# Performance work log

Measured on AMD Instinct MI355X. Metric: run time of the kernel, lower is better.

The kernel has to match this reference:

```python
import jax, jax.numpy as jnp
import numpy as np

N, K, D_INT, D_EXT = 10000, 16, 8, 16
D = 128          # node_representation_size
V_INT = 50000    # unique_internal_nodes
B = 2048


def _xavier(key, shape):
    fan_in, fan_out = shape[-1], shape[-2] if len(shape) > 1 else shape[-1]
    std = float(np.sqrt(2.0 / (fan_in + fan_out)))
    return jax.random.normal(key, shape, dtype=jnp.float32) * std


def setup_inputs() -> dict:
    key = jax.random.key(0)
    ks = jax.random.split(key, 16)
    batch = jax.random.randint(ks[0], (B, 2), 0, N)
    int_node_ids = jax.random.randint(ks[1], (N, K), 0, V_INT)
    int_neigh_ids = jax.random.randint(ks[2], (N, K, D_INT), 0, V_INT)
    ext_neigh = jax.random.randint(ks[3], (N, D_EXT), 0, N)
    E = jax.random.normal(ks[4], (V_INT, D), dtype=jnp.float32)  # nn.Embedding default init
    W = _xavier(ks[5], (D, D))
    M = _xavier(ks[6], (D, D))
    U = _xavier(ks[7], (D, D))
    V = _xavier(ks[8], (D, D))
    W1 = _xavier(ks[9], (D, 2 * D))
    b1 = jnp.zeros((D,), dtype=jnp.float32)
    W2 = _xavier(ks[10], (2, D))
    b2 = jnp.zeros((2,), dtype=jnp.float32)
    return {"batch": batch, "int_node_ids": int_node_ids,
            "int_neigh_ids": int_neigh_ids, "ext_neigh": ext_neigh,
            "E": E, "W": W, "M": M, "U": U, "V": V,
            "W1": W1, "b1": b1, "W2": W2, "b2": b2}


def reference(batch, int_node_ids, int_neigh_ids, ext_neigh,
              E, W, M, U, V, W1, b1, W2, b2):
    # --- InternalGraphConvolutionLayer, vectorized over all N external nodes ---
    emb = E[int_node_ids]                          # (N, K, d) per-internal-node embedding
    nb_sum = E[int_neigh_ids].sum(axis=2)          # (N, K, d) sum of internal neighbours
    # sum_k = relu(W @ e_k + M @ sum_j e_j)
    s = jax.nn.relu(jnp.einsum('ij,nkj->nki', W, emb)
                    + jnp.einsum('ij,nkj->nki', M, nb_sum))
    r = s.sum(axis=1)                              # (N, d) accumulate over internal nodes
    h = jax.nn.softmax(r, axis=-1)                 # softmax over dim 0 of the (d,1) column

    # --- ExternalGraphConvolutionLayer ---
    ext_sum = h[ext_neigh].sum(axis=1)             # (N, d)
    e_all = jax.nn.softmax(
        jax.nn.relu(jnp.einsum('ij,nj->ni', U, h)
                    + jnp.einsum('ij,nj->ni', V, ext_sum)), axis=-1)  # (N, d)

    # --- LinkPredictionLayer over batch pairs ---
    ea = e_all[batch[:, 0]]                        # (B, d)
    eb = e_all[batch[:, 1]]                        # (B, d)
    x = jnp.concatenate([ea, eb], axis=-1)         # (B, 2d)
    x = jax.nn.leaky_relu(x @ W1.T + b1)           # (B, d), slope 0.01 as in F.leaky_relu
    logits = x @ W2.T + b2                         # (B, 2)
    return jax.nn.softmax(logits, axis=-1)
```

## Files before the change

### kernel.cpp

```cpp
#include <hip/hip_runtime.h>
#include <hip/hip_fp16.h>

#define VINT 50000
#define NN   10000
#define KK   16
#define DINT 8
#define DEXT 16
#define DD   128
#define BB   2048

typedef __attribute__((ext_vector_type(8))) short  bf16x8;
typedef __attribute__((ext_vector_type(4))) short  short4v;
typedef __attribute__((ext_vector_type(4))) float  f32x4;

struct __align__(8)  half4 { __half2 a, b; };
struct __align__(16) half8 { __half2 a, b, c, d; };

__device__ inline short bf_rne(float f) {
    unsigned u = __float_as_uint(f);
    return (short)((u + 0x7FFFu + ((u >> 16) & 1u)) >> 16);
}

__device__ inline void store_acc(__half* p, f32x4 v) {
    half4 h;
    h.a = __floats2half2_rn(v[0], v[1]);
    h.b = __floats2half2_rn(v[2], v[3]);
    *(half4*)p = h;
}
__device__ inline void store_acc(float* p, f32x4 v) {
    *(float4*)p = make_float4(v[0], v[1], v[2], v[3]);
}

__global__ __launch_bounds__(256) void k_convert(
    const float* __restrict__ src, short* __restrict__ dst, int n4)
{
    int i = blockIdx.x * 256 + threadIdx.x;
    if (i >= n4) return;
    float4 v = ((const float4*)src)[i];
    short4v o = {bf_rne(v.x), bf_rne(v.y), bf_rne(v.z), bf_rne(v.w)};
    ((short4v*)dst)[i] = o;
}

__global__ __launch_bounds__(256) void k_convert_mats(
    const float* __restrict__ W, const float* __restrict__ M,
    const float* __restrict__ U, const float* __restrict__ V,
    const float* __restrict__ W1,
    short* __restrict__ WMbf, short* __restrict__ UVbf,
    short* __restrict__ W1bf)
{
    int bid = blockIdx.x;
    if (bid < 64) {
        int which = bid >> 4;
        int i = (bid & 15) * 256 + threadIdx.x;
        const float* src = (which == 0) ? W : (which == 1) ? M : (which == 2) ? U : V;
        short* dst = (which < 2) ? WMbf : UVbf;
        int off = (which & 1) * (DD * DD / 4);
        float4 v = ((const float4*)src)[i];
        short4v o = {bf_rne(v.x), bf_rne(v.y), bf_rne(v.z), bf_rne(v.w)};
        ((short4v*)dst)[off + i] = o;
    } else {
        int i = (bid - 64) * 256 + threadIdx.x;
        float4 v = ((const float4*)W1)[i];
        short4v o = {bf_rne(v.x), bf_rne(v.y), bf_rne(v.z), bf_rne(v.w)};
        ((short4v*)W1bf)[i] = o;
    }
}

template <typename OutT>
__global__ __launch_bounds__(256, 2) void k_mfma_dual(
    const short* __restrict__ Xbf, const short* __restrict__ ABbf,
    OutT* __restrict__ OA, OutT* __restrict__ OB, int nrows)
{
    const int n0 = blockIdx.x * 64;
    const int w  = threadIdx.x >> 6;
    const int l  = threadIdx.x & 63;
    const int lr = l & 15;
    const int lk = l >> 4;

    f32x4 acc[4][4];
    #pragma unroll
    for (int mi = 0; mi < 4; ++mi)
        #pragma unroll
        for (int ni = 0; ni < 4; ++ni)
            acc[mi][ni] = (f32x4){0.f, 0.f, 0.f, 0.f};

    const bf16x8 zf = {0, 0, 0, 0, 0, 0, 0, 0};

    for (int ks = 0; ks < 4; ++ks) {
        const int kb = ks * 32 + lk * 8;
        bf16x8 ah[4], bh[4];
        #pragma unroll
        for (int mi = 0; mi < 4; ++mi) {
            int m = w * 64 + mi * 16 + lr;
            ah[mi] = *(const bf16x8*)&ABbf[m * DD + kb];
        }
        #pragma unroll
        for (int ni = 0; ni < 4; ++ni) {
            int n = n0 + ni * 16 + lr;
            bh[ni] = (n < nrows) ? *(const bf16x8*)&Xbf[(size_t)n * DD + kb] : zf;
        }
        #pragma unroll
        for (int mi = 0; mi < 4; ++mi)
            #pragma unroll
            for (int ni = 0; ni < 4; ++ni)
                acc[mi][ni] = __builtin_amdgcn_mfma_f32_16x16x32_bf16(ah[mi], bh[ni], acc[mi][ni], 0, 0, 0);
    }

    #pragma unroll
    for (int ni = 0; ni < 4; ++ni) {
        int n = n0 + ni * 16 + lr;
        if (n >= nrows) continue;
        #pragma unroll
        for (int mi = 0; mi < 4; ++mi) {
            int m = w * 64 + mi * 16 + lk * 4;
            if (m < DD) store_acc(&OA[(size_t)n * DD + m], acc[mi][ni]);
            else        store_acc(&OB[(size_t)n * DD + (m - DD)], acc[mi][ni]);
        }
    }
}

__global__ __launch_bounds__(256, 7) void k_node(
    const int* __restrict__ node_ids, const int* __restrict__ neigh_ids,
    const __half* __restrict__ WE, const __half* __restrict__ ME,
    short* __restrict__ Hbf)
{
    __shared__ int idx[4][KK * (1 + DINT)];
    const int t  = threadIdx.x;
    const int n0 = blockIdx.x * 4;

    if (t < 4 * KK) idx[t >> 4][t & 15] = node_ids[n0 * KK + t];
    for (int x = t; x < 4 * KK * DINT; x += 256)
        idx[x >> 7][KK + (x & 127)] = neigh_ids[n0 * KK * DINT + x];
    __syncthreads();

    const int w   = t >> 6;
    const int l   = t & 63;
    const int g16 = l >> 4;
    const int p   = l & 15;
    const int n   = n0 + w;
    const int* ids = idx[w];

    float r[8] = {0.f, 0.f, 0.f, 0.f, 0.f, 0.f, 0.f, 0.f};
    #pragma unroll
    for (int kk = 0; kk < 4; ++kk) {
        const int k = kk * 4 + g16;
        half8 rw = *(const half8*)(WE + (size_t)ids[k] * DD + p * 8);
        half8 rm[DINT];
        #pragma unroll
        for (int e = 0; e < DINT; ++e)
            rm[e] = *(const half8*)(ME + (size_t)ids[KK + k * DINT + e] * DD + p * 8);

        float2 f0 = __half22float2(rw.a), f1 = __half22float2(rw.b);
        float2 f2 = __half22float2(rw.c), f3 = __half22float2(rw.d);
        float s[8] = {f0.x, f0.y, f1.x, f1.y, f2.x, f2.y, f3.x, f3.y};
        #pragma unroll
        for (int e = 0; e < DINT; ++e) {
            float2 m0 = __half22float2(rm[e].a), m1 = __half22float2(rm[e].b);
            float2 m2 = __half22float2(rm[e].c), m3 = __half22float2(rm[e].d);
            s[0] += m0.x; s[1] += m0.y; s[2] += m1.x; s[3] += m1.y;
            s[4] += m2.x; s[5] += m2.y; s[6] += m3.x; s[7] += m3.y;
        }
        #pragma unroll
        for (int j = 0; j < 8; ++j) r[j] += fmaxf(s[j], 0.f);
    }

    #pragma unroll
    for (int j = 0; j < 8; ++j) {
        r[j] += __shfl_xor(r[j], 16);
        r[j] += __shfl_xor(r[j], 32);
    }

    float mx = r[0];
    #pragma unroll
    for (int j = 1; j < 8; ++j) mx = fmaxf(mx, r[j]);
    #pragma unroll
    for (int off = 8; off >= 1; off >>= 1) mx = fmaxf(mx, __shfl_xor(mx, off));
    float e[8], sum = 0.f;
    #pragma unroll
    for (int j = 0; j < 8; ++j) { e[j] = expf(r[j] - mx); sum += e[j]; }
    #pragma unroll
    for (int off = 8; off >= 1; off >>= 1) sum += __shfl_xor(sum, off);
    float inv = 1.f / sum;
    if (g16 == 0) {
        bf16x8 o = {bf_rne(e[0] * inv), bf_rne(e[1] * inv), bf_rne(e[2] * inv), bf_rne(e[3] * inv),
                    bf_rne(e[4] * inv), bf_rne(e[5] * inv), bf_rne(e[6] * inv), bf_rne(e[7] * inv)};
        *(bf16x8*)(Hbf + (size_t)n * DD + p * 8) = o;
    }
}

__global__ __launch_bounds__(256) void k_ext2(
    const int* __restrict__ ext_neigh, const __half* __restrict__ UH,
    const __half* __restrict__ VH, float* __restrict__ EALL)
{
    __shared__ int idx[4][DEXT];
    const int t  = threadIdx.x;
    const int n0 = blockIdx.x * 4;
    if (t < 4 * DEXT) idx[t >> 4][t & 15] = ext_neigh[n0 * DEXT + t];
    __syncthreads();

    const int w  = t >> 6;
    const int l  = t & 63;
    const int c  = l & 31;
    const int hf = l >> 5;
    const int n  = n0 + w;

    float sx = 0.f, sy = 0.f, sz = 0.f, sw = 0.f;
    if (hf == 0) {
        half4 a = *(const half4*)(UH + (size_t)n * DD + 4 * c);
        float2 a0 = __half22float2(a.a), a1 = __half22float2(a.b);
        sx = a0.x; sy = a0.y; sz = a1.x; sw = a1.y;
    }
    #pragma unroll
    for (int jj = 0; jj < 8; ++jj) {
        half4 v = *(const half4*)(VH + (size_t)idx[w][hf * 8 + jj] * DD + 4 * c);
        float2 v0 = __half22float2(v.a), v1 = __half22float2(v.b);
        sx += v0.x; sy += v0.y; sz += v1.x; sw += v1.y;
    }
    sx += __shfl_xor(sx, 32); sy += __shfl_xor(sy, 32);
    sz += __shfl_xor(sz, 32); sw += __shfl_xor(sw, 32);

    sx = fmaxf(sx, 0.f); sy = fmaxf(sy, 0.f);
    sz = fmaxf(sz, 0.f); sw = fmaxf(sw, 0.f);

    float mx = fmaxf(fmaxf(sx, sy), fmaxf(sz, sw));
    #pragma unroll
    for (int off = 16; off >= 1; off >>= 1) mx = fmaxf(mx, __shfl_xor(mx, off));
    float ex = expf(sx - mx), ey = expf(sy - mx), ez = expf(sz - mx), ew = expf(sw - mx);
    float s = ex + ey + ez + ew;
    #pragma unroll
    for (int off = 16; off >= 1; off >>= 1) s += __shfl_xor(s, off);
    float inv = 1.f / s;
    if (hf == 0)
        *(float4*)(EALL + (size_t)n * DD + 4 * c) = make_float4(ex * inv, ey * inv, ez * inv, ew * inv);
}

__global__ __launch_bounds__(256) void k_mlp_mfma(
    const int* __restrict__ batch, const float* __restrict__ EA,
    const short* __restrict__ W1bf, const float* __restrict__ b1,
    const float* __restrict__ W2, const float* __restrict__ b2,
    float* __restrict__ out)
{
    __shared__ int pidx[128];
    __shared__ float red0[4][64];
    __shared__ float red1[4][64];
    const int t = threadIdx.x, w = t >> 6, l = t & 63;
    const int lr = l & 15, lk = l >> 4;
    const int b0 = blockIdx.x * 64;

    if (t < 128) pidx[t] = batch[b0 * 2 + t];
    __syncthreads();

    f32x4 acc[2][4];
    #pragma unroll
    for (int mi = 0; mi < 2; ++mi)
        #pragma unroll
        for (int ni = 0; ni < 4; ++ni)
            acc[mi][ni] = (f32x4){0.f, 0.f, 0.f, 0.f};

    for (int ks = 0; ks < 8; ++ks) {
        const int kb = ks * 32 + lk * 8;
        const int sel = (ks >= 4);
        const int koff = kb - sel * 128;
        bf16x8 ah[2], bh[4];
        #pragma unroll
        for (int mi = 0; mi < 2; ++mi) {
            int m = w * 32 + mi * 16 + lr;
            ah[mi] = *(const bf16x8*)&W1bf[m * (2 * DD) + kb];
        }
        #pragma unroll
        for (int ni = 0; ni < 4; ++ni) {
            int n = ni * 16 + lr;
            int row = pidx[2 * n + sel];
            float4 v0 = *(const float4*)&EA[(size_t)row * DD + koff];
            float4 v1 = *(const float4*)&EA[(size_t)row * DD + koff + 4];
            bf16x8 tmp = {bf_rne(v0.x), bf_rne(v0.y), bf_rne(v0.z), bf_rne(v0.w),
                          bf_rne(v1.x), bf_rne(v1.y), bf_rne(v1.z), bf_rne(v1.w)};
            bh[ni] = tmp;
        }
        #pragma unroll
        for (int mi = 0; mi < 2; ++mi)
            #pragma unroll
            for (int ni = 0; ni < 4; ++ni)
                acc[mi][ni] = __builtin_amdgcn_mfma_f32_16x16x32_bf16(ah[mi], bh[ni], acc[mi][ni], 0, 0, 0);
    }

    float bb[2][4], w2a[2][4], w2b[2][4];
    #pragma unroll
    for (int mi = 0; mi < 2; ++mi)
        #pragma unroll
        for (int rr = 0; rr < 4; ++rr) {
            int m = w * 32 + mi * 16 + lk * 4 + rr;
            bb[mi][rr]  = b1[m];
            w2a[mi][rr] = W2[m];
            w2b[mi][rr] = W2[DD + m];
        }

    #pragma unroll
    for (int ni = 0; ni < 4; ++ni) {
        float p0 = 0.f, p1 = 0.f;
        #pragma unroll
        for (int mi = 0; mi < 2; ++mi)
            #pragma unroll
            for (int rr = 0; rr < 4; ++rr) {
                float x = acc[mi][ni][rr] + bb[mi][rr];
                x = (x > 0.f) ? x : 0.01f * x;
                p0 = fmaf(w2a[mi][rr], x, p0);
                p1 = fmaf(w2b[mi][rr], x, p1);
            }
        p0 += __shfl_xor(p0, 16); p0 += __shfl_xor(p0, 32);
        p1 += __shfl_xor(p1, 16); p1 += __shfl_xor(p1, 32);
        if (lk == 0) {
            red0[w][ni * 16 + lr] = p0;
            red1[w][ni * 16 + lr] = p1;
        }
    }
    __syncthreads();
    if (t < 64) {
        float l0 = red0[0][t] + red0[1][t] + red0[2][t] + red0[3][t] + b2[0];
        float l1 = red1[0][t] + red1[1][t] + red1[2][t] + red1[3][t] + b2[1];
        float mm = fmaxf(l0, l1);
        float e0 = expf(l0 - mm), e1 = expf(l1 - mm);
        float inv = 1.f / (e0 + e1);
        out[2 * (b0 + t)]     = e0 * inv;
        out[2 * (b0 + t) + 1] = e1 * inv;
    }
}

extern "C" void kernel_launch(void* const* d_in, const int* in_sizes, int n_in,
                              void* d_out, int out_size, void* d_ws, size_t ws_size,
                              hipStream_t stream) {
    const int*   batch     = (const int*)d_in[0];
    const int*   node_ids  = (const int*)d_in[1];
    const int*   neigh_ids = (const int*)d_in[2];
    const int*   ext_neigh = (const int*)d_in[3];
    const float* E         = (const float*)d_in[4];
    const float* W         = (const float*)d_in[5];
    const float* M         = (const float*)d_in[6];
    const float* U         = (const float*)d_in[7];
    const float* V         = (const float*)d_in[8];
    const float* W1        = (const float*)d_in[9];
    const float* b1        = (const float*)d_in[10];
    const float* W2        = (const float*)d_in[11];
    const float* b2        = (const float*)d_in[12];

    __half* WE   = (__half*)d_ws;
    __half* ME   = WE + (size_t)VINT * DD;
    short*  Ebf  = (short*)(ME + (size_t)VINT * DD);
    short*  Hbf  = Ebf + (size_t)VINT * DD;
    short*  WMbf = Hbf + (size_t)NN * DD;
    short*  UVbf = WMbf + 256 * DD;
    short*  W1bf = UVbf + 256 * DD;
    __half* UHh  = (__half*)(W1bf + DD * 2 * DD);
    __half* VHh  = UHh + (size_t)NN * DD;
    float*  EA   = (float*)(VHh + (size_t)NN * DD);
    float*  out  = (float*)d_out;

    k_convert<<<(VINT * DD / 4 + 255) / 256, 256, 0, stream>>>(E, Ebf, VINT * DD / 4);
    k_convert_mats<<<96, 256, 0, stream>>>(W, M, U, V, W1, WMbf, UVbf, W1bf);
    k_mfma_dual<__half><<<(VINT + 63) / 64, 256, 0, stream>>>(Ebf, WMbf, WE, ME, VINT);
    k_node<<<NN / 4, 256, 0, stream>>>(node_ids, neigh_ids, WE, ME, Hbf);
    k_mfma_dual<__half><<<(NN + 63) / 64, 256, 0, stream>>>(Hbf, UVbf, UHh, VHh, NN);
    k_ext2<<<NN / 4, 256, 0, stream>>>(ext_neigh, UHh, VHh, EA);
    k_mlp_mfma<<<BB / 64, 256, 0, stream>>>(batch, EA, W1bf, b1, W2, b2, out);
}
```

Baseline: 105.4 us.

## Fuse fp32-to-bf16 conversion of E into the dual MFMA GEMM

```diff
diff --git a/kernel.cpp b/kernel.cpp
--- a/kernel.cpp
+++ b/kernel.cpp
@@ -1,5 +1,6 @@
 #include <hip/hip_runtime.h>
 #include <hip/hip_fp16.h>
+#include <hip/hip_bf16.h>
 
 #define VINT 50000
 #define NN   10000
@@ -21,6 +22,15 @@
     return (short)((u + 0x7FFFu + ((u >> 16) & 1u)) >> 16);
 }
 
+__device__ inline bf16x8 cvt8_bf16(float4 a, float4 b) {
+    union { __hip_bfloat162 h2[4]; bf16x8 v; } u;
+    u.h2[0] = __float22bfloat162_rn(make_float2(a.x, a.y));
+    u.h2[1] = __float22bfloat162_rn(make_float2(a.z, a.w));
+    u.h2[2] = __float22bfloat162_rn(make_float2(b.x, b.y));
+    u.h2[3] = __float22bfloat162_rn(make_float2(b.z, b.w));
+    return u.v;
+}
+
 __device__ inline void store_acc(__half* p, f32x4 v) {
     half4 h;
     h.a = __floats2half2_rn(v[0], v[1]);
@@ -29,16 +39,6 @@
 }
 __device__ inline void store_acc(float* p, f32x4 v) {
     *(float4*)p = make_float4(v[0], v[1], v[2], v[3]);
-}
-
-__global__ __launch_bounds__(256) void k_convert(
-    const float* __restrict__ src, short* __restrict__ dst, int n4)
-{
-    int i = blockIdx.x * 256 + threadIdx.x;
-    if (i >= n4) return;
-    float4 v = ((const float4*)src)[i];
-    short4v o = {bf_rne(v.x), bf_rne(v.y), bf_rne(v.z), bf_rne(v.w)};
-    ((short4v*)dst)[i] = o;
 }
 
 __global__ __launch_bounds__(256) void k_convert_mats(
@@ -67,8 +67,8 @@
 }
 
 template <typename OutT>
-__global__ __launch_bounds__(256, 2) void k_mfma_dual(
-    const short* __restrict__ Xbf, const short* __restrict__ ABbf,
+__global__ __launch_bounds__(256, 2) void k_mfma_dual_f32(
+    const float* __restrict__ X, const short* __restrict__ ABbf,
     OutT* __restrict__ OA, OutT* __restrict__ OB, int nrows)
 {
     const int n0 = blockIdx.x * 64;
@@ -84,8 +84,24 @@
         for (int ni = 0; ni < 4; ++ni)
             acc[mi][ni] = (f32x4){0.f, 0.f, 0.f, 0.f};
 
-    const bf16x8 zf = {0, 0, 0, 0, 0, 0, 0, 0};
-
+    const float4 zf4 = make_float4(0.f, 0.f, 0.f, 0.f);
+    int nrow[4];
+    #pragma unroll
+    for (int ni = 0; ni < 4; ++ni) nrow[ni] = n0 + ni * 16 + lr;
+
+    float4 bv0[4], bv1[4];
+    auto loadB = [&](int ks) {
+        const int kb = ks * 32 + lk * 8;
+        #pragma unroll
+        for (int ni = 0; ni < 4; ++ni) {
+            if (nrow[ni] < nrows) {
+                bv0[ni] = *(const float4*)&X[(size_t)nrow[ni] * DD + kb];
+                bv1[ni] = *(const float4*)&X[(size_t)nrow[ni] * DD + kb + 4];
+            } else { bv0[ni] = zf4; bv1[ni] = zf4; }
+        }
+    };
+
+    loadB(0);
     for (int ks = 0; ks < 4; ++ks) {
         const int kb = ks * 32 + lk * 8;
         bf16x8 ah[4], bh[4];
@@ -95,10 +111,9 @@
             ah[mi] = *(const bf16x8*)&ABbf[m * DD + kb];
         }
         #pragma unroll
-        for (int ni = 0; ni < 4; ++ni) {
-            int n = n0 + ni * 16 + lr;
-            bh[ni] = (n < nrows) ? *(const bf16x8*)&Xbf[(size_t)n * DD + kb] : zf;
-        }
+        for (int ni = 0; ni < 4; ++ni)
+            bh[ni] = cvt8_bf16(bv0[ni], bv1[ni]);
+        if (ks < 3) loadB(ks + 1);
         #pragma unroll
         for (int mi = 0; mi < 4; ++mi)
             #pragma unroll
@@ -108,7 +123,7 @@
 
     #pragma unroll
     for (int ni = 0; ni < 4; ++ni) {
-        int n = n0 + ni * 16 + lr;
+        int n = nrow[ni];
         if (n >= nrows) continue;
         #pragma unroll
         for (int mi = 0; mi < 4; ++mi) {
@@ -119,7 +134,60 @@
     }
 }
 
-__global__ __launch_bounds__(256, 7) void k_node(
+template <typename OutT>
+__global__ __launch_bounds__(256, 2) void k_mfma_dual(
+    const short* __restrict__ Xbf, const short* __restrict__ ABbf,
+    OutT* __restrict__ OA, OutT* __restrict__ OB, int nrows)
+{
+    const int n0 = blockIdx.x * 64;
+    const int w  = threadIdx.x >> 6;
+    const int l  = threadIdx.x & 63;
+    const int lr = l & 15;
+    const int lk = l >> 4;
+
+    f32x4 acc[4][4];
+    #pragma unroll
+    for (int mi = 0; mi < 4; ++mi)
+        #pragma unroll
+        for (int ni = 0; ni < 4; ++ni)
+            acc[mi][ni] = (f32x4){0.f, 0.f, 0.f, 0.f};
+
+    const bf16x8 zf = {0, 0, 0, 0, 0, 0, 0, 0};
+
+    for (int ks = 0; ks < 4; ++ks) {
+        const int kb = ks * 32 + lk * 8;
+        bf16x8 ah[4], bh[4];
+        #pragma unroll
+        for (int mi = 0; mi < 4; ++mi) {
+            int m = w * 64 + mi * 16 + lr;
+            ah[mi] = *(const bf16x8*)&ABbf[m * DD + kb];
+        }
+        #pragma unroll
+        for (int ni = 0; ni < 4; ++ni) {
+            int n = n0 + ni * 16 + lr;
+            bh[ni] = (n < nrows) ? *(const bf16x8*)&Xbf[(size_t)n * DD + kb] : zf;
+        }
+        #pragma unroll
+        for (int mi = 0; mi < 4; ++mi)
+            #pragma unroll
+            for (int ni = 0; ni < 4; ++ni)
+                acc[mi][ni] = __builtin_amdgcn_mfma_f32_16x16x32_bf16(ah[mi], bh[ni], acc[mi][ni], 0, 0, 0);
+    }
+
+    #pragma unroll
+    for (int ni = 0; ni < 4; ++ni) {
+        int n = n0 + ni * 16 + lr;
+        if (n >= nrows) continue;
+        #pragma unroll
+        for (int mi = 0; mi < 4; ++mi) {
+            int m = w * 64 + mi * 16 + lk * 4;
+            if (m < DD) store_acc(&OA[(size_t)n * DD + m], acc[mi][ni]);
+            else        store_acc(&OB[(size_t)n * DD + (m - DD)], acc[mi][ni]);
+        }
+    }
+}
+
+__global__ __launch_bounds__(256) void k_node(
     const int* __restrict__ node_ids, const int* __restrict__ neigh_ids,
     const __half* __restrict__ WE, const __half* __restrict__ ME,
     short* __restrict__ Hbf)
@@ -273,9 +341,7 @@
             int row = pidx[2 * n + sel];
             float4 v0 = *(const float4*)&EA[(size_t)row * DD + koff];
             float4 v1 = *(const float4*)&EA[(size_t)row * DD + koff + 4];
-            bf16x8 tmp = {bf_rne(v0.x), bf_rne(v0.y), bf_rne(v0.z), bf_rne(v0.w),
-                          bf_rne(v1.x), bf_rne(v1.y), bf_rne(v1.z), bf_rne(v1.w)};
-            bh[ni] = tmp;
+            bh[ni] = cvt8_bf16(v0, v1);
         }
         #pragma unroll
         for (int mi = 0; mi < 2; ++mi)
@@ -345,8 +411,7 @@
 
     __half* WE   = (__half*)d_ws;
     __half* ME   = WE + (size_t)VINT * DD;
-    short*  Ebf  = (short*)(ME + (size_t)VINT * DD);
-    short*  Hbf  = Ebf + (size_t)VINT * DD;
+    short*  Hbf  = (short*)(ME + (size_t)VINT * DD);
     short*  WMbf = Hbf + (size_t)NN * DD;
     short*  UVbf = WMbf + 256 * DD;
     short*  W1bf = UVbf + 256 * DD;
@@ -355,9 +420,8 @@
     float*  EA   = (float*)(VHh + (size_t)NN * DD);
     float*  out  = (float*)d_out;
 
-    k_convert<<<(VINT * DD / 4 + 255) / 256, 256, 0, stream>>>(E, Ebf, VINT * DD / 4);
     k_convert_mats<<<96, 256, 0, stream>>>(W, M, U, V, W1, WMbf, UVbf, W1bf);
-    k_mfma_dual<__half><<<(VINT + 63) / 64, 256, 0, stream>>>(Ebf, WMbf, WE, ME, VINT);
+    k_mfma_dual_f32<__half><<<(VINT + 63) / 64, 256, 0, stream>>>(E, WMbf, WE, ME, VINT);
     k_node<<<NN / 4, 256, 0, stream>>>(node_ids, neigh_ids, WE, ME, Hbf);
     k_mfma_dual<__half><<<(NN + 63) / 64, 256, 0, stream>>>(Hbf, UVbf, UHh, VHh, NN);
     k_ext2<<<NN / 4, 256, 0, stream>>>(ext_neigh, UHh, VHh, EA);
```

After: 109.1 us. +3.5%, slower.

## Chunk WE/ME tables by column slab and split node gather from softmax

Applied to the files above, without the earlier changes.

```diff
diff --git a/kernel.cpp b/kernel.cpp
--- a/kernel.cpp
+++ b/kernel.cpp
@@ -1,5 +1,6 @@
 #include <hip/hip_runtime.h>
 #include <hip/hip_fp16.h>
+#include <hip/hip_bf16.h>
 
 #define VINT 50000
 #define NN   10000
@@ -8,6 +9,9 @@
 #define DEXT 16
 #define DD   128
 #define BB   2048
+#define CW   16
+#define NCH  8
+#define NPB  64
 
 typedef __attribute__((ext_vector_type(8))) short  bf16x8;
 typedef __attribute__((ext_vector_type(4))) short  short4v;
@@ -19,6 +23,15 @@
 __device__ inline short bf_rne(float f) {
     unsigned u = __float_as_uint(f);
     return (short)((u + 0x7FFFu + ((u >> 16) & 1u)) >> 16);
+}
+
+__device__ inline bf16x8 cvt8_bf16(float4 a, float4 b) {
+    union { __hip_bfloat162 h2[4]; bf16x8 v; } u;
+    u.h2[0] = __float22bfloat162_rn(make_float2(a.x, a.y));
+    u.h2[1] = __float22bfloat162_rn(make_float2(a.z, a.w));
+    u.h2[2] = __float22bfloat162_rn(make_float2(b.x, b.y));
+    u.h2[3] = __float22bfloat162_rn(make_float2(b.z, b.w));
+    return u.v;
 }
 
 __device__ inline void store_acc(__half* p, f32x4 v) {
@@ -66,7 +79,7 @@
     }
 }
 
-template <typename OutT>
+template <typename OutT, bool CHUNK>
 __global__ __launch_bounds__(256, 2) void k_mfma_dual(
     const short* __restrict__ Xbf, const short* __restrict__ ABbf,
     OutT* __restrict__ OA, OutT* __restrict__ OB, int nrows)
@@ -113,78 +126,85 @@
         #pragma unroll
         for (int mi = 0; mi < 4; ++mi) {
             int m = w * 64 + mi * 16 + lk * 4;
-            if (m < DD) store_acc(&OA[(size_t)n * DD + m], acc[mi][ni]);
-            else        store_acc(&OB[(size_t)n * DD + (m - DD)], acc[mi][ni]);
-        }
-    }
-}
-
-__global__ __launch_bounds__(256, 7) void k_node(
+            OutT* P = (m < DD) ? OA : OB;
+            int mm = (m < DD) ? m : m - DD;
+            if (CHUNK) {
+                size_t off = ((size_t)(mm >> 4) * nrows + n) * CW + (mm & 15);
+                store_acc(&P[off], acc[mi][ni]);
+            } else {
+                store_acc(&P[(size_t)n * DD + mm], acc[mi][ni]);
+            }
+        }
+    }
+}
+
+__global__ __launch_bounds__(256) void k_node_gather(
     const int* __restrict__ node_ids, const int* __restrict__ neigh_ids,
-    const __half* __restrict__ WE, const __half* __restrict__ ME,
-    short* __restrict__ Hbf)
-{
-    __shared__ int idx[4][KK * (1 + DINT)];
+    const __half* __restrict__ WEc, const __half* __restrict__ MEc,
+    float* __restrict__ Rbuf)
+{
+    __shared__ int idxn[NPB][KK];
+    __shared__ int idxg[NPB][KK * DINT];
+    const int c  = blockIdx.x & (NCH - 1);
+    const int nb = blockIdx.x >> 3;
     const int t  = threadIdx.x;
-    const int n0 = blockIdx.x * 4;
-
-    if (t < 4 * KK) idx[t >> 4][t & 15] = node_ids[n0 * KK + t];
-    for (int x = t; x < 4 * KK * DINT; x += 256)
-        idx[x >> 7][KK + (x & 127)] = neigh_ids[n0 * KK * DINT + x];
+
+    for (int x = t; x < NPB * KK; x += 256) {
+        int node = x >> 4, r = x & 15;
+        int gn = nb * NPB + node;
+        idxn[node][r] = (gn < NN) ? node_ids[gn * KK + r] : 0;
+    }
+    for (int x = t; x < NPB * KK * DINT; x += 256) {
+        int node = x >> 7, r = x & 127;
+        int gn = nb * NPB + node;
+        idxg[node][r] = (gn < NN) ? neigh_ids[gn * KK * DINT + r] : 0;
+    }
     __syncthreads();
 
-    const int w   = t >> 6;
-    const int l   = t & 63;
-    const int g16 = l >> 4;
-    const int p   = l & 15;
-    const int n   = n0 + w;
-    const int* ids = idx[w];
-
-    float r[8] = {0.f, 0.f, 0.f, 0.f, 0.f, 0.f, 0.f, 0.f};
-    #pragma unroll
-    for (int kk = 0; kk < 4; ++kk) {
-        const int k = kk * 4 + g16;
-        half8 rw = *(const half8*)(WE + (size_t)ids[k] * DD + p * 8);
-        half8 rm[DINT];
-        #pragma unroll
-        for (int e = 0; e < DINT; ++e)
-            rm[e] = *(const half8*)(ME + (size_t)ids[KK + k * DINT + e] * DD + p * 8);
-
-        float2 f0 = __half22float2(rw.a), f1 = __half22float2(rw.b);
-        float2 f2 = __half22float2(rw.c), f3 = __half22float2(rw.d);
-        float s[8] = {f0.x, f0.y, f1.x, f1.y, f2.x, f2.y, f3.x, f3.y};
+    const int nl = t >> 2;
+    const int q  = t & 3;
+    const int n  = nb * NPB + nl;
+    const __half* WEb = WEc + (size_t)c * VINT * CW + 4 * q;
+    const __half* MEb = MEc + (size_t)c * VINT * CW + 4 * q;
+
+    float r0 = 0.f, r1 = 0.f, r2 = 0.f, r3 = 0.f;
+    #pragma unroll 4
+    for (int k = 0; k < KK; ++k) {
+        half4 wv = *(const half4*)(WEb + (size_t)idxn[nl][k] * CW);
+        float2 a0 = __half22float2(wv.a), a1 = __half22float2(wv.b);
+        float s0 = a0.x, s1 = a0.y, s2 = a1.x, s3 = a1.y;
         #pragma unroll
         for (int e = 0; e < DINT; ++e) {
-            float2 m0 = __half22float2(rm[e].a), m1 = __half22float2(rm[e].b);
-            float2 m2 = __half22float2(rm[e].c), m3 = __half22float2(rm[e].d);
-            s[0] += m0.x; s[1] += m0.y; s[2] += m1.x; s[3] += m1.y;
-            s[4] += m2.x; s[5] += m2.y; s[6] += m3.x; s[7] += m3.y;
-        }
-        #pragma unroll
-        for (int j = 0; j < 8; ++j) r[j] += fmaxf(s[j], 0.f);
-    }
-
-    #pragma unroll
-    for (int j = 0; j < 8; ++j) {
-        r[j] += __shfl_xor(r[j], 16);
-        r[j] += __shfl_xor(r[j], 32);
-    }
-
-    float mx = r[0];
-    #pragma unroll
-    for (int j = 1; j < 8; ++j) mx = fmaxf(mx, r[j]);
-    #pragma unroll
-    for (int off = 8; off >= 1; off >>= 1) mx = fmaxf(mx, __shfl_xor(mx, off));
-    float e[8], sum = 0.f;
-    #pragma unroll
-    for (int j = 0; j < 8; ++j) { e[j] = expf(r[j] - mx); sum += e[j]; }
-    #pragma unroll
-    for (int off = 8; off >= 1; off >>= 1) sum += __shfl_xor(sum, off);
-    float inv = 1.f / sum;
-    if (g16 == 0) {
-        bf16x8 o = {bf_rne(e[0] * inv), bf_rne(e[1] * inv), bf_rne(e[2] * inv), bf_rne(e[3] * inv),
-                    bf_rne(e[4] * inv), bf_rne(e[5] * inv), bf_rne(e[6] * inv), bf_rne(e[7] * inv)};
-        *(bf16x8*)(Hbf + (size_t)n * DD + p * 8) = o;
+            half4 mv = *(const half4*)(MEb + (size_t)idxg[nl][k * DINT + e] * CW);
+            float2 b0 = __half22float2(mv.a), b1 = __half22float2(mv.b);
+            s0 += b0.x; s1 += b0.y; s2 += b1.x; s3 += b1.y;
+        }
+        r0 += fmaxf(s0, 0.f); r1 += fmaxf(s1, 0.f);
+        r2 += fmaxf(s2, 0.f); r3 += fmaxf(s3, 0.f);
+    }
+    if (n < NN)
+        *(float4*)(Rbuf + (size_t)n * DD + c * CW + 4 * q) = make_float4(r0, r1, r2, r3);
+}
+
+__global__ __launch_bounds__(256) void k_node_softmax(
+    const float* __restrict__ Rbuf, short* __restrict__ Hbf)
+{
+    const int t = threadIdx.x;
+    const int w = t >> 6, l = t & 63;
+    const int cc = l & 31;
+    const int n = blockIdx.x * 4 + w;
+    float4 v = *(const float4*)(Rbuf + (size_t)n * DD + 4 * cc);
+    float mx = fmaxf(fmaxf(v.x, v.y), fmaxf(v.z, v.w));
+    #pragma unroll
+    for (int off = 16; off >= 1; off >>= 1) mx = fmaxf(mx, __shfl_xor(mx, off));
+    float e0 = expf(v.x - mx), e1 = expf(v.y - mx), e2 = expf(v.z - mx), e3 = expf(v.w - mx);
+    float s = e0 + e1 + e2 + e3;
+    #pragma unroll
+    for (int off = 16; off >= 1; off >>= 1) s += __shfl_xor(s, off);
+    float inv = 1.f / s;
+    if (l < 32) {
+        short4v o = {bf_rne(e0 * inv), bf_rne(e1 * inv), bf_rne(e2 * inv), bf_rne(e3 * inv)};
+        *(short4v*)(Hbf + (size_t)n * DD + 4 * cc) = o;
     }
 }
 
@@ -273,9 +293,7 @@
             int row = pidx[2 * n + sel];
             float4 v0 = *(const float4*)&EA[(size_t)row * DD + koff];
             float4 v1 = *(const float4*)&EA[(size_t)row * DD + koff + 4];
-            bf16x8 tmp = {bf_rne(v0.x), bf_rne(v0.y), bf_rne(v0.z), bf_rne(v0.w),
-                          bf_rne(v1.x), bf_rne(v1.y), bf_rne(v1.z), bf_rne(v1.w)};
-            bh[ni] = tmp;
+            bh[ni] = cvt8_bf16(v0, v1);
         }
         #pragma unroll
         for (int mi = 0; mi < 2; ++mi)
@@ -343,10 +361,11 @@
     const float* W2        = (const float*)d_in[11];
     const float* b2        = (const float*)d_in[12];
 
-    __half* WE   = (__half*)d_ws;
-    __half* ME   = WE + (size_t)VINT * DD;
-    short*  Ebf  = (short*)(ME + (size_t)VINT * DD);
-    short*  Hbf  = Ebf + (size_t)VINT * DD;
+    __half* WEc  = (__half*)d_ws;
+    __half* MEc  = WEc + (size_t)VINT * DD;
+    short*  Ebf  = (short*)(MEc + (size_t)VINT * DD);
+    float*  Rbuf = (float*)(Ebf + (size_t)VINT * DD);
+    short*  Hbf  = (short*)(Rbuf + (size_t)NN * DD);
     short*  WMbf = Hbf + (size_t)NN * DD;
     short*  UVbf = WMbf + 256 * DD;
     short*  W1bf = UVbf + 256 * DD;
@@ -355,11 +374,14 @@
     float*  EA   = (float*)(VHh + (size_t)NN * DD);
     float*  out  = (float*)d_out;
 
+    const int NB = (NN + NPB - 1) / NPB;
+
     k_convert<<<(VINT * DD / 4 + 255) / 256, 256, 0, stream>>>(E, Ebf, VINT * DD / 4);
     k_convert_mats<<<96, 256, 0, stream>>>(W, M, U, V, W1, WMbf, UVbf, W1bf);
-    k_mfma_dual<__half><<<(VINT + 63) / 64, 256, 0, stream>>>(Ebf, WMbf, WE, ME, VINT);
-    k_node<<<NN / 4, 256, 0, stream>>>(node_ids, neigh_ids, WE, ME, Hbf);
-    k_mfma_dual<__half><<<(NN + 63) / 64, 256, 0, stream>>>(Hbf, UVbf, UHh, VHh, NN);
+    k_mfma_dual<__half, true><<<(VINT + 63) / 64, 256, 0, stream>>>(Ebf, WMbf, WEc, MEc, VINT);
+    k_node_gather<<<NCH * NB, 256, 0, stream>>>(node_ids, neigh_ids, WEc, MEc, Rbuf);
+    k_node_softmax<<<NN / 4, 256, 0, stream>>>(Rbuf, Hbf);
+    k_mfma_dual<__half, false><<<(NN + 63) / 64, 256, 0, stream>>>(Hbf, UVbf, UHh, VHh, NN);
     k_ext2<<<NN / 4, 256, 0, stream>>>(ext_neigh, UHh, VHh, EA);
     k_mlp_mfma<<<BB / 64, 256, 0, stream>>>(batch, EA, W1bf, b1, W2, b2, out);
 }
```

New measurement: 154.3 us. +46.4%, slower.
